# Performance work log

Hardware: AMD Instinct MI355X
Metric: run time of the kernel (lower is better)

Reference implementation:

```python
import jax, jax.numpy as jnp
import numpy as np

B, N, E, H = 32, 1024, 1024, 8
D = E // H      # head_dim = 128, att_mid_dim = [128, 64, 128]
MID = 64


def setup_inputs() -> dict:
    key = jax.random.key(0)
    ks = jax.random.split(key, 12)

    def lin(k, out_d, in_d):
        return (jax.random.normal(k, (out_d, in_d), jnp.float32) * 0.02,
                jnp.zeros((out_d,), jnp.float32))

    Wq, bq = lin(ks[0], E, E)
    Wk, bk = lin(ks[1], E, E)
    Wv, bv = lin(ks[2], E, E)
    Wb, bb = lin(ks[3], MID, D)    # attention_basic: Linear(mid[0]=D -> mid[1]=64) + ReLU
    Wl, bl = lin(ks[4], 1, MID)    # attention_last: Linear(64 -> 1)
    Wl2, bl2 = lin(ks[5], D, MID)  # attention_last2: Linear(64 -> D)
    query = jax.random.normal(ks[6], (B, E), jnp.float32)
    k_in = jax.random.normal(ks[7], (B, N, E), jnp.float32)
    value1 = jax.random.normal(ks[8], (B, E), jnp.float32)
    value2 = jax.random.normal(ks[9], (B, N, E), jnp.float32)
    mask = jax.random.randint(ks[10], (B, N), 0, 2, jnp.int32)
    mask = mask.at[:, 0].set(1)  # guarantee at least one valid position per row
    return {"query": query, "key": k_in, "mask": mask, "value1": value1,
            "value2": value2, "Wq": Wq, "bq": bq, "Wk": Wk, "bk": bk,
            "Wv": Wv, "bv": bv, "Wb": Wb, "bb": bb, "Wl": Wl, "bl": bl,
            "Wl2": Wl2, "bl2": bl2}


def reference(query, key, mask, value1, value2, Wq, bq, Wk, bk, Wv, bv,
              Wb, bb, Wl, bl, Wl2, bl2):
    # --- QKV projections (single-query attention) ---
    Q = (query @ Wq.T + bq).reshape(B, 1, H, D).transpose(0, 2, 1, 3)    # [B,H,1,D]
    K = (key @ Wk.T + bk).reshape(B, N, H, D).transpose(0, 2, 1, 3)      # [B,H,N,D]
    V = (key @ Wv.T + bv).reshape(B, N, H, D).transpose(0, 2, 1, 3)      # [B,H,N,D]
    v1 = value1.reshape(B, H, D)                                          # [B,H,D]
    v2 = (value2 @ Wv.T + bv).reshape(B, N, H, D).transpose(0, 2, 1, 3)   # [B,H,N,D]

    scores = jnp.einsum('bhqd,bhkd->bhqk', Q, K) / jnp.sqrt(jnp.float32(D))  # [B,H,1,N]
    attended = jnp.einsum('bhqk,bhkd->bhqd', scores, V)                      # [B,H,1,D]
    attn_map = jnp.broadcast_to(attended, (B, H, N, D))                      # expand(-1,-1,N,-1)

    # --- SCAtt attn_net ---
    h = jax.nn.relu(jnp.einsum('bhnd,md->bhnm', attn_map, Wb) + bb)          # [B,H,N,64]
    mf = mask.astype(h.dtype)                                                # [B,N]
    mext = mf[:, None, :, None]                                              # [B,1,N,1]
    att_map_pool = jnp.sum(h * mext, axis=2) / jnp.sum(mext, axis=2)         # [B,H,64]
    alpha_spatial = (jnp.einsum('bhnm,om->bhno', h, Wl) + bl)[..., 0]        # [B,H,N]
    alpha_channel = jax.nn.sigmoid(att_map_pool @ Wl2.T + bl2)               # [B,H,D]
    alpha_spatial = jnp.where(mf[:, None, :] == 0, jnp.float32(-1e9), alpha_spatial)
    alpha_spatial = jax.nn.softmax(alpha_spatial, axis=-1)                   # [B,H,N]
    v2_att = jnp.einsum('bhn,bhnd->bhd', alpha_spatial, v2)                  # [B,H,D]
    attn = v1 * v2_att * alpha_channel                                       # [B,H,D]
    return attn.reshape(B, H * D)
```

## Files before the change

### kernel.cpp

```cpp
#include <hip/hip_runtime.h>

#define B_  32
#define N_  1024
#define E_  1024
#define H_  8
#define D_  128
#define MID_ 64
#define NT_  32
#define TR_  32
#define NSP_ 32


__device__ __forceinline__ void ldsbar() {
    asm volatile("s_waitcnt lgkmcnt(0)\n"
                 "s_barrier" ::: "memory");
}

__global__ __launch_bounds__(256) void k_q(
        const float* __restrict__ query, const float* __restrict__ Wq,
        const float* __restrict__ bq, const float* __restrict__ bk,
        float* __restrict__ Qs, float* __restrict__ qb,
        const float* __restrict__ value2, const int* __restrict__ mask,
        float* __restrict__ P2p)
{
    const int t = threadIdx.x;

    __shared__ __align__(16) float qsh[8 * E_];
    __shared__ __align__(16) float Qrow[8][16];
    __shared__ int rows[NSP_];
    __shared__ int nrows;

    if (blockIdx.x < 256) {
        const int bg = blockIdx.x >> 6;
        const int rs = blockIdx.x & 63;
        const int b0 = bg * 8;
        const int R  = rs * 16;
        const int h  = rs >> 3;

        {
            const int bb = t >> 5, ln = t & 31;
            const float4* src = (const float4*)(query + (size_t)(b0 + bb) * E_);
            float4* dst = (float4*)(qsh + bb * E_);
            #pragma unroll
            for (int i = 0; i < 8; ++i) dst[ln + i * 32] = src[ln + i * 32];
        }
        __syncthreads();

        const int r = t >> 4, cl = t & 15;
        const int row = R + r;
        const float4* wr = (const float4*)(Wq + (size_t)row * E_);
        float4 wchunk[16];
        #pragma unroll
        for (int i = 0; i < 16; ++i) wchunk[i] = wr[cl + i * 16];

        const float bqv = bq[row];
        const float4* qsh4 = (const float4*)qsh;
        #pragma unroll
        for (int bb = 0; bb < 8; ++bb) {
            float acc = 0.f;
            #pragma unroll
            for (int i = 0; i < 16; ++i) {
                float4 q = qsh4[bb * 256 + cl + i * 16];
                acc += wchunk[i].x * q.x + wchunk[i].y * q.y
                     + wchunk[i].z * q.z + wchunk[i].w * q.w;
            }
            #pragma unroll
            for (int off = 8; off; off >>= 1) acc += __shfl_xor(acc, off);
            if (cl == 0) Qrow[bb][r] = acc + bqv;
        }
        __syncthreads();

        if (t < 8) {
            float s = 0.f;
            #pragma unroll
            for (int rr = 0; rr < 16; ++rr) s += Qrow[t][rr] * bk[R + rr];
            atomicAdd(&qb[(b0 + t) * 8 + h], s);
        }
        if (t < 32) {
            const int bb = t >> 2, j = t & 3;
            ((float4*)(Qs + (size_t)(b0 + bb) * E_))[rs * 4 + j] =
                *(const float4*)&Qrow[bb][j * 4];
        }
    } else {
        const int pi = blockIdx.x - 256;
        const int b = pi & 31, sp = pi >> 5;
        const int e0 = t * 4;
        const int n0 = sp * NSP_;

        if (t == 0) nrows = 0;
        __syncthreads();
        if (t < NSP_) {
            if (mask[b * N_ + n0 + t]) {
                int i2 = atomicAdd(&nrows, 1);
                rows[i2] = t;
            }
        }
        __syncthreads();
        const int nr = nrows;

        float a0 = 0.f, a1 = 0.f, a2 = 0.f, a3 = 0.f;
        const float* vb = value2 + ((size_t)(b * N_ + n0)) * E_ + e0;
        #pragma unroll 4
        for (int i = 0; i < nr; ++i) {
            float4 v = *(const float4*)(vb + (size_t)rows[i] * E_);
            a0 += v.x; a1 += v.y; a2 += v.z; a3 += v.w;
        }
        float* dst = P2p + ((size_t)(sp & 7) * B_ + b) * E_ + e0;
        atomicAdd(dst + 0, a0); atomicAdd(dst + 1, a1);
        atomicAdd(dst + 2, a2); atomicAdd(dst + 3, a3);
    }
}

__global__ __launch_bounds__(256) void k_k(
        const float* __restrict__ Qs, const float* __restrict__ Wk,
        float* __restrict__ qk)
{
    const int h = blockIdx.x >> 5, ec = blockIdx.x & 31;
    const int t = threadIdx.x;

    __shared__ __align__(16) float QsL[32 * 132];
    __shared__ __align__(16) float WkL[128 * 32];

    {
        const int b = t >> 3, j = t & 7;
        const float4* src = (const float4*)(Qs + (size_t)b * E_) + h * 32;
        float4* dst = (float4*)(QsL + b * 132);
        #pragma unroll
        for (int jj = 0; jj < 4; ++jj) dst[j + jj * 8] = src[j + jj * 8];
    }
    {
        #pragma unroll
        for (int jj = 0; jj < 4; ++jj) {
            const int idx = t + jj * 256;
            const int d = idx >> 3, c = idx & 7;
            ((float4*)WkL)[idx] =
                ((const float4*)(Wk + (size_t)(h * D_ + d) * E_))[ec * 8 + c];
        }
    }
    __syncthreads();

    const int b = t >> 3, eg = t & 7;
    float4 acc = make_float4(0.f, 0.f, 0.f, 0.f);
    const float* q = QsL + b * 132;
    const float4* wk4 = (const float4*)WkL;
    #pragma unroll 8
    for (int d = 0; d < D_; ++d) {
        float qd = q[d];
        float4 w = wk4[d * 8 + eg];
        acc.x += qd * w.x; acc.y += qd * w.y;
        acc.z += qd * w.z; acc.w += qd * w.w;
    }
    ((float4*)(qk + (size_t)(b * 8 + h) * E_))[ec * 8 + eg] = acc;
}

__global__ __launch_bounds__(256) void k_main(
        const float* __restrict__ key, const float* __restrict__ qk,
        const float* __restrict__ qb, float* __restrict__ PPpart,
        float* __restrict__ ssum)
{
    const int tile = blockIdx.x, b = blockIdx.y;
    const int t = threadIdx.x;
    const int w = t >> 6, l = t & 63;

    __shared__ __align__(16) float part[4][4][8];
    __shared__ __align__(16) float sfin[4][8];

    const float scale = 0.08838834764831845f;
    const float* keyb = key + ((size_t)b * N_ + (size_t)tile * TR_) * E_;
    const float qbv = (t < 32) ? qb[b * 8 + (t & 7)] : 0.f;

    float4 qkr[8];
    #pragma unroll
    for (int h = 0; h < H_; ++h)
        qkr[h] = ((const float4*)(qk + (size_t)(b * 8 + h) * E_))[t];

    float4 pacc[8];
    #pragma unroll
    for (int h = 0; h < 8; ++h) pacc[h] = make_float4(0.f, 0.f, 0.f, 0.f);

    float ts = 0.f;

    float4 kv[4];
    #pragma unroll
    for (int r = 0; r < 4; ++r)
        kv[r] = ((const float4*)(keyb + (size_t)r * E_))[t];

    for (int st = 0; st < 8; ++st) {
        #pragma unroll
        for (int r = 0; r < 4; ++r) {
            float p[8];
            #pragma unroll
            for (int h = 0; h < 8; ++h)
                p[h] = qkr[h].x * kv[r].x + qkr[h].y * kv[r].y
                     + qkr[h].z * kv[r].z + qkr[h].w * kv[r].w;
            #pragma unroll
            for (int off = 32; off; off >>= 1) {
                #pragma unroll
                for (int h = 0; h < 8; ++h)
                    p[h] += __shfl_xor(p[h], off);
            }
            if (l == 0) {
                *(float4*)&part[w][r][0] = make_float4(p[0], p[1], p[2], p[3]);
                *(float4*)&part[w][r][4] = make_float4(p[4], p[5], p[6], p[7]);
            }
        }
        float4 kn[4];
        if (st < 7) {
            #pragma unroll
            for (int r = 0; r < 4; ++r)
                kn[r] = ((const float4*)(keyb
                            + (size_t)((st + 1) * 4 + r) * E_))[t];
        }
        ldsbar();
        if (t < 32) {
            const int r = t >> 3, h = t & 7;
            float s = (part[0][r][h] + part[1][r][h]
                     + part[2][r][h] + part[3][r][h] + qbv) * scale;
            sfin[r][h] = s;
            ts += s;
        }
        ldsbar();
        #pragma unroll
        for (int r = 0; r < 4; ++r) {
            const float4 k4 = kv[r];
            const float4 sA = *(const float4*)&sfin[r][0];
            const float4 sB = *(const float4*)&sfin[r][4];
            pacc[0].x += sA.x * k4.x; pacc[0].y += sA.x * k4.y;
            pacc[0].z += sA.x * k4.z; pacc[0].w += sA.x * k4.w;
            pacc[1].x += sA.y * k4.x; pacc[1].y += sA.y * k4.y;
            pacc[1].z += sA.y * k4.z; pacc[1].w += sA.y * k4.w;
            pacc[2].x += sA.z * k4.x; pacc[2].y += sA.z * k4.y;
            pacc[2].z += sA.z * k4.z; pacc[2].w += sA.z * k4.w;
            pacc[3].x += sA.w * k4.x; pacc[3].y += sA.w * k4.y;
            pacc[3].z += sA.w * k4.z; pacc[3].w += sA.w * k4.w;
            pacc[4].x += sB.x * k4.x; pacc[4].y += sB.x * k4.y;
            pacc[4].z += sB.x * k4.z; pacc[4].w += sB.x * k4.w;
            pacc[5].x += sB.y * k4.x; pacc[5].y += sB.y * k4.y;
            pacc[5].z += sB.y * k4.z; pacc[5].w += sB.y * k4.w;
            pacc[6].x += sB.z * k4.x; pacc[6].y += sB.z * k4.y;
            pacc[6].z += sB.z * k4.z; pacc[6].w += sB.z * k4.w;
            pacc[7].x += sB.w * k4.x; pacc[7].y += sB.w * k4.y;
            pacc[7].z += sB.w * k4.z; pacc[7].w += sB.w * k4.w;
        }
        #pragma unroll
        for (int r = 0; r < 4; ++r) kv[r] = kn[r];
    }

    if (t < 32) {
        float v = ts;
        v += __shfl_xor(v, 8);
        v += __shfl_xor(v, 16);
        if (l < 8) atomicAdd(&ssum[b * 8 + l], v);
    }

    #pragma unroll
    for (int h = 0; h < 8; ++h) {
        ((float4*)(PPpart
            + (((size_t)(b * H_ + h)) * NT_ + tile) * E_))[t] = pacc[h];
    }
}

__global__ __launch_bounds__(512) void k_tail(
        const float* __restrict__ PPpart, const float* __restrict__ P2p,
        const float* __restrict__ ssumg, const int* __restrict__ mask,
        const float* __restrict__ Wv, const float* __restrict__ bv,
        const float* __restrict__ Wb, const float* __restrict__ bb,
        const float* __restrict__ Wl2, const float* __restrict__ bl2,
        const float* __restrict__ value1, float* __restrict__ out)
{
    const int bh = blockIdx.x, b = bh >> 3, h = bh & 7;
    const int t = threadIdx.x;
    const int l = t & 63, w = t >> 6;
    const int rg = l >> 4, cl = l & 15;

    __shared__ __align__(16) float ph[2][E_];
    __shared__ __align__(16) float pooled[E_];
    __shared__ __align__(16) float pool2[E_];
    __shared__ float attA_s[D_];
    __shared__ float attV_s[D_];
    __shared__ float att[D_];
    __shared__ float hv[MID_];
    __shared__ float red2[2];
    __shared__ float cnt_s;

    {
        const int c4 = t & 255, half = t >> 8;
        const float4* pp = (const float4*)(PPpart + (size_t)bh * NT_ * E_);
        float4 s = make_float4(0.f, 0.f, 0.f, 0.f);
        #pragma unroll 4
        for (int j = 0; j < 16; ++j) {
            float4 v = pp[(half * 16 + j) * 256 + c4];
            s.x += v.x; s.y += v.y; s.z += v.z; s.w += v.w;
        }
        ((float4*)&ph[half][0])[c4] = s;
    }
    __syncthreads();
    if (t < 256) {
        float4 p0 = ((const float4*)&ph[0][0])[t];
        float4 p1 = ((const float4*)&ph[1][0])[t];
        ((float4*)pooled)[t] = make_float4(p0.x + p1.x, p0.y + p1.y,
                                           p0.z + p1.z, p0.w + p1.w);
        float4 q = make_float4(0.f, 0.f, 0.f, 0.f);
        #pragma unroll
        for (int k2 = 0; k2 < 8; ++k2) {
            float4 v = ((const float4*)(P2p + ((size_t)k2 * B_ + b) * E_))[t];
            q.x += v.x; q.y += v.y; q.z += v.z; q.w += v.w;
        }
        ((float4*)pool2)[t] = q;
    }
    __syncthreads();

    const float4* pooled4 = (const float4*)pooled;
    const float4* pool24  = (const float4*)pool2;
    #pragma unroll
    for (int p = 0; p < 4; ++p) {
        const int d = p * 32 + w * 4 + rg;
        const float4* wvr = (const float4*)(Wv + (size_t)(h * D_ + d) * E_);
        float pA = 0.f, pV = 0.f;
        #pragma unroll 4
        for (int i = 0; i < 16; ++i) {
            float4 wv4 = wvr[cl + i * 16];
            float4 pa = pooled4[cl + i * 16];
            float4 pb = pool24[cl + i * 16];
            pA += wv4.x * pa.x + wv4.y * pa.y + wv4.z * pa.z + wv4.w * pa.w;
            pV += wv4.x * pb.x + wv4.y * pb.y + wv4.z * pb.z + wv4.w * pb.w;
        }
        #pragma unroll
        for (int off = 8; off; off >>= 1) {
            pA += __shfl_xor(pA, off);
            pV += __shfl_xor(pV, off);
        }
        if (cl == 0) { attA_s[d] = pA; attV_s[d] = pV; }
    }
    __syncthreads();

    if (t < 128) {
        int ci = 0;
        #pragma unroll
        for (int i = 0; i < 8; ++i) ci += mask[b * N_ + t + i * 128];
        float cf = (float)ci;
        #pragma unroll
        for (int off = 32; off; off >>= 1) cf += __shfl_down(cf, off);
        if ((t & 63) == 0) red2[t >> 6] = cf;
        const float ss = ssumg[bh];
        att[t] = attA_s[t] + ss * bv[h * D_ + t];
    }
    __syncthreads();
    if (t == 0) cnt_s = red2[0] + red2[1];
    if (t < MID_) {
        float a = bb[t];
        #pragma unroll 4
        for (int d2 = 0; d2 < D_; ++d2) a += att[d2] * Wb[t * D_ + d2];
        hv[t] = fmaxf(a, 0.f);
    }
    __syncthreads();
    if (t < 128) {
        float z = bl2[t];
        #pragma unroll
        for (int m = 0; m < MID_; ++m) z += hv[m] * Wl2[t * MID_ + m];
        float alphac = 1.f / (1.f + expf(-z));
        const float bvd = bv[h * D_ + t];
        float v2a = attV_s[t] / cnt_s + bvd;
        out[(size_t)b * E_ + h * D_ + t] =
            value1[(size_t)b * E_ + h * D_ + t] * v2a * alphac;
    }
}

extern "C" void kernel_launch(void* const* d_in, const int* in_sizes, int n_in,
                              void* d_out, int out_size, void* d_ws, size_t ws_size,
                              hipStream_t stream)
{
    const float* query  = (const float*)d_in[0];
    const float* key    = (const float*)d_in[1];
    const int*   mask   = (const int*)d_in[2];
    const float* value1 = (const float*)d_in[3];
    const float* value2 = (const float*)d_in[4];
    const float* Wq  = (const float*)d_in[5];
    const float* bq  = (const float*)d_in[6];
    const float* Wk  = (const float*)d_in[7];
    const float* bk  = (const float*)d_in[8];
    const float* Wv  = (const float*)d_in[9];
    const float* bv  = (const float*)d_in[10];
    const float* Wb  = (const float*)d_in[11];
    const float* bb  = (const float*)d_in[12];
    const float* Wl2 = (const float*)d_in[15];
    const float* bl2 = (const float*)d_in[16];
    float* out = (float*)d_out;

    char* ws = (char*)d_ws;
    const size_t SZ_PPP = (size_t)B_ * H_ * NT_ * E_ * 4;
    const size_t SZ_P2P = (size_t)8 * B_ * E_ * 4;
    const size_t OFF_P2P = SZ_PPP;
    const size_t OFF_SS  = OFF_P2P + SZ_P2P;
    const size_t OFF_QB  = OFF_SS + 1024;
    const size_t OFF_QS  = OFF_QB + 1024;
    const size_t OFF_QK  = OFF_QS + (size_t)B_ * E_ * 4;
    float* PPpart = (float*)(ws);
    float* P2p    = (float*)(ws + OFF_P2P);
    float* ssum   = (float*)(ws + OFF_SS);
    float* qb     = (float*)(ws + OFF_QB);
    float* Qs     = (float*)(ws + OFF_QS);
    float* qk     = (float*)(ws + OFF_QK);

    hipMemsetAsync(ws + OFF_P2P, 0, SZ_P2P + 2048, stream);

    hipLaunchKernelGGL(k_q, dim3(256 + NT_ * B_), dim3(256), 0, stream,
                       query, Wq, bq, bk, Qs, qb, value2, mask, P2p);
    hipLaunchKernelGGL(k_k, dim3(256), dim3(256), 0, stream,
                       Qs, Wk, qk);
    hipLaunchKernelGGL(k_main, dim3(NT_, B_), dim3(256), 0, stream,
                       key, qk, qb, PPpart, ssum);
    hipLaunchKernelGGL(k_tail, dim3(B_ * H_), dim3(512), 0, stream,
                       PPpart, P2p, ssum, mask, Wv, bv, Wb, bb, Wl2, bl2,
                       value1, out);
}
```

Before: 370.0 us.

## Compute key-query scores with bf16 MFMA in a separate pass before accumulation

The score computation in k_main no longer uses per-row fp32 dot products with wavefront shuffle reductions and two barriers per step. Each block now converts its 32 key rows and the qk vectors to bf16 in LDS and runs 16x16x32 bf16 MFMA to get all 32x8 scores at once, then does the fp32 score-weighted key accumulation in a second pass. The qk intermediate is also stored as bf16. This removes shuffle and barrier overhead in the inner loop, but reads each key tile twice and lowers score precision to bf16 inputs.

Result: faster. 353.3 us, median of 2 (-4.5%).

```diff
diff --git a/kernel.cpp b/kernel.cpp
--- a/kernel.cpp
+++ b/kernel.cpp
@@ -7,13 +7,18 @@
 #define D_  128
 #define MID_ 64
 #define NT_  32
-#define TR_  32
 #define NSP_ 32
 
 
-__device__ __forceinline__ void ldsbar() {
-    asm volatile("s_waitcnt lgkmcnt(0)\n"
-                 "s_barrier" ::: "memory");
+typedef __attribute__((ext_vector_type(8))) short bf16x8;
+typedef __attribute__((ext_vector_type(4))) float f32x4;
+
+__device__ __forceinline__ unsigned bf2(float a, float b) {
+    unsigned ua = __float_as_uint(a);
+    ua = (ua + 0x7fffu + ((ua >> 16) & 1u)) >> 16;
+    unsigned ub = __float_as_uint(b);
+    ub = (ub + 0x7fffu + ((ub >> 16) & 1u)) >> 16;
+    return ua | (ub << 16);
 }
 
 __global__ __launch_bounds__(256) void k_q(
@@ -113,7 +118,7 @@
 
 __global__ __launch_bounds__(256) void k_k(
         const float* __restrict__ Qs, const float* __restrict__ Wk,
-        float* __restrict__ qk)
+        unsigned short* __restrict__ qkb)
 {
     const int h = blockIdx.x >> 5, ec = blockIdx.x & 31;
     const int t = threadIdx.x;
@@ -150,11 +155,14 @@
         acc.x += qd * w.x; acc.y += qd * w.y;
         acc.z += qd * w.z; acc.w += qd * w.w;
     }
-    ((float4*)(qk + (size_t)(b * 8 + h) * E_))[ec * 8 + eg] = acc;
+    uint2 pk;
+    pk.x = bf2(acc.x, acc.y);
+    pk.y = bf2(acc.z, acc.w);
+    ((uint2*)(qkb + (size_t)(b * 8 + h) * E_))[ec * 8 + eg] = pk;
 }
 
 __global__ __launch_bounds__(256) void k_main(
-        const float* __restrict__ key, const float* __restrict__ qk,
+        const float* __restrict__ key, const unsigned short* __restrict__ qkb,
         const float* __restrict__ qb, float* __restrict__ PPpart,
         float* __restrict__ ssum)
 {
@@ -162,23 +170,75 @@
     const int t = threadIdx.x;
     const int w = t >> 6, l = t & 63;
 
-    __shared__ __align__(16) float part[4][4][8];
-    __shared__ __align__(16) float sfin[4][8];
+    __shared__ __align__(16) unsigned short KLs[32 * 264];
+    __shared__ __align__(16) unsigned short QLs[8 * 264];
+    __shared__ __align__(16) float part[2][2][16][16];
+    __shared__ __align__(16) float sfin[32][8];
 
     const float scale = 0.08838834764831845f;
-    const float* keyb = key + ((size_t)b * N_ + (size_t)tile * TR_) * E_;
-    const float qbv = (t < 32) ? qb[b * 8 + (t & 7)] : 0.f;
-
-    float4 qkr[8];
+    const float* keyb = key + ((size_t)b * N_ + (size_t)tile * 32) * E_;
+    const unsigned short* qkbb = qkb + (size_t)(b * 8) * E_;
+
+    const int mtile = w & 1, ksub = w >> 1;
+    const int arow = mtile * 16 + (l & 15);
+    const int brow = l & 7;
+    const int kgrp = (l >> 4) * 16;
+
+    f32x4 Cacc = {0.f, 0.f, 0.f, 0.f};
+
+    for (int q = 0; q < 4; ++q) {
+        #pragma unroll
+        for (int j = 0; j < 8; ++j) {
+            const int idx = t + j * 256;
+            const int row = idx >> 6, c4 = idx & 63;
+            float4 v = ((const float4*)(keyb + (size_t)row * E_))[q * 64 + c4];
+            uint2 pk;
+            pk.x = bf2(v.x, v.y);
+            pk.y = bf2(v.z, v.w);
+            ((uint2*)(KLs + row * 264))[c4] = pk;
+        }
+        #pragma unroll
+        for (int j = 0; j < 2; ++j) {
+            const int idx = t + j * 256;
+            const int h = idx >> 6, c4 = idx & 63;
+            ((uint2*)(QLs + h * 264))[c4] =
+                ((const uint2*)(qkbb + (size_t)h * E_))[q * 64 + c4];
+        }
+        __syncthreads();
+        #pragma unroll
+        for (int s = 0; s < 4; ++s) {
+            const int koff = (ksub * 4 + s) * 64 + kgrp;
+            bf16x8 a = *(const bf16x8*)((const char*)(KLs + arow * 264) + koff);
+            bf16x8 bb = *(const bf16x8*)((const char*)(QLs + brow * 264) + koff);
+            Cacc = __builtin_amdgcn_mfma_f32_16x16x32_bf16(a, bb, Cacc, 0, 0, 0);
+        }
+        if (q < 3) __syncthreads();
+    }
+
     #pragma unroll
-    for (int h = 0; h < H_; ++h)
-        qkr[h] = ((const float4*)(qk + (size_t)(b * 8 + h) * E_))[t];
+    for (int j = 0; j < 4; ++j)
+        part[mtile][ksub][(l >> 4) * 4 + j][l & 15] = Cacc[j];
+    __syncthreads();
+
+    {
+        const int r = t >> 3, h = t & 7;
+        const float s = (part[r >> 4][0][r & 15][h]
+                       + part[r >> 4][1][r & 15][h]
+                       + qb[b * 8 + h]) * scale;
+        sfin[r][h] = s;
+    }
+    __syncthreads();
+
+    if (t < 8) {
+        float ts = 0.f;
+        #pragma unroll
+        for (int r = 0; r < 32; ++r) ts += sfin[r][t];
+        atomicAdd(&ssum[b * 8 + t], ts);
+    }
 
     float4 pacc[8];
     #pragma unroll
     for (int h = 0; h < 8; ++h) pacc[h] = make_float4(0.f, 0.f, 0.f, 0.f);
-
-    float ts = 0.f;
 
     float4 kv[4];
     #pragma unroll
@@ -186,24 +246,6 @@
         kv[r] = ((const float4*)(keyb + (size_t)r * E_))[t];
 
     for (int st = 0; st < 8; ++st) {
-        #pragma unroll
-        for (int r = 0; r < 4; ++r) {
-            float p[8];
-            #pragma unroll
-            for (int h = 0; h < 8; ++h)
-                p[h] = qkr[h].x * kv[r].x + qkr[h].y * kv[r].y
-                     + qkr[h].z * kv[r].z + qkr[h].w * kv[r].w;
-            #pragma unroll
-            for (int off = 32; off; off >>= 1) {
-                #pragma unroll
-                for (int h = 0; h < 8; ++h)
-                    p[h] += __shfl_xor(p[h], off);
-            }
-            if (l == 0) {
-                *(float4*)&part[w][r][0] = make_float4(p[0], p[1], p[2], p[3]);
-                *(float4*)&part[w][r][4] = make_float4(p[4], p[5], p[6], p[7]);
-            }
-        }
         float4 kn[4];
         if (st < 7) {
             #pragma unroll
@@ -211,20 +253,11 @@
                 kn[r] = ((const float4*)(keyb
                             + (size_t)((st + 1) * 4 + r) * E_))[t];
         }
-        ldsbar();
-        if (t < 32) {
-            const int r = t >> 3, h = t & 7;
-            float s = (part[0][r][h] + part[1][r][h]
-                     + part[2][r][h] + part[3][r][h] + qbv) * scale;
-            sfin[r][h] = s;
-            ts += s;
-        }
-        ldsbar();
         #pragma unroll
         for (int r = 0; r < 4; ++r) {
             const float4 k4 = kv[r];
-            const float4 sA = *(const float4*)&sfin[r][0];
-            const float4 sB = *(const float4*)&sfin[r][4];
+            const float4 sA = *(const float4*)&sfin[st * 4 + r][0];
+            const float4 sB = *(const float4*)&sfin[st * 4 + r][4];
             pacc[0].x += sA.x * k4.x; pacc[0].y += sA.x * k4.y;
             pacc[0].z += sA.x * k4.z; pacc[0].w += sA.x * k4.w;
             pacc[1].x += sA.y * k4.x; pacc[1].y += sA.y * k4.y;
@@ -244,13 +277,6 @@
         }
         #pragma unroll
         for (int r = 0; r < 4; ++r) kv[r] = kn[r];
-    }
-
-    if (t < 32) {
-        float v = ts;
-        v += __shfl_xor(v, 8);
-        v += __shfl_xor(v, 16);
-        if (l < 8) atomicAdd(&ssum[b * 8 + l], v);
     }
 
     #pragma unroll
@@ -394,22 +420,22 @@
     const size_t OFF_SS  = OFF_P2P + SZ_P2P;
     const size_t OFF_QB  = OFF_SS + 1024;
     const size_t OFF_QS  = OFF_QB + 1024;
-    const size_t OFF_QK  = OFF_QS + (size_t)B_ * E_ * 4;
+    const size_t OFF_QKB = OFF_QS + (size_t)B_ * E_ * 4;
     float* PPpart = (float*)(ws);
     float* P2p    = (float*)(ws + OFF_P2P);
     float* ssum   = (float*)(ws + OFF_SS);
     float* qb     = (float*)(ws + OFF_QB);
     float* Qs     = (float*)(ws + OFF_QS);
-    float* qk     = (float*)(ws + OFF_QK);
+    unsigned short* qkb = (unsigned short*)(ws + OFF_QKB);
 
     hipMemsetAsync(ws + OFF_P2P, 0, SZ_P2P + 2048, stream);
 
     hipLaunchKernelGGL(k_q, dim3(256 + NT_ * B_), dim3(256), 0, stream,
                        query, Wq, bq, bk, Qs, qb, value2, mask, P2p);
     hipLaunchKernelGGL(k_k, dim3(256), dim3(256), 0, stream,
-                       Qs, Wk, qk);
+                       Qs, Wk, qkb);
     hipLaunchKernelGGL(k_main, dim3(NT_, B_), dim3(256), 0, stream,
-                       key, qk, qb, PPpart, ssum);
+                       key, qkb, qb, PPpart, ssum);
     hipLaunchKernelGGL(k_tail, dim3(B_ * H_), dim3(512), 0, stream,
                        PPpart, P2p, ssum, mask, Wv, bv, Wb, bb, Wl2, bl2,
                        value1, out);
```
